# Kernel optimization log

Measured on AMD Instinct MI355X. Metric: run time of the kernel, lower is better.

## Reference

```python
import jax, jax.numpy as jnp
import numpy as np

ALPHA = 1.702   # swiglu_alpha
LIMIT = 7.0     # swiglu_limit
EPS = 1e-5      # norm_eps
E = 16          # num_experts
K = 4           # experts_per_token


def _swiglu(h):
    # interleaved split as in torch: even cols -> glu, odd cols -> linear
    x_glu = jnp.minimum(h[..., ::2], LIMIT)
    # faithful to source bug: clamp(min=limit, max=limit) == constant limit
    x_lin = jnp.clip(h[..., 1::2], LIMIT, LIMIT)
    return x_glu * jax.nn.sigmoid(ALPHA * x_glu) * (x_lin + 1.0)


def setup_inputs() -> dict:
    key = jax.random.key(0)
    ks = jax.random.split(key, 7)
    B, T, H, I = 1, 2048, 1024, 1024
    x = jax.random.normal(ks[0], (B, T, H), jnp.float32)
    scale = jnp.ones((H,), jnp.float32)
    gate_w = jax.random.normal(ks[1], (E, H), jnp.float32) * 0.02
    gate_b = jnp.zeros((E,), jnp.float32)
    mlp1_w = jax.random.normal(ks[2], (E, 2 * I, H), jnp.float32) * 0.02
    mlp1_b = jax.random.normal(ks[3], (E, 2 * I), jnp.float32) * 0.02
    mlp2_w = jax.random.normal(ks[4], (E, H, I), jnp.float32) * 0.02
    mlp2_b = jax.random.normal(ks[5], (E, H), jnp.float32) * 0.02
    return dict(x=x, scale=scale, gate_w=gate_w, gate_b=gate_b,
                mlp1_w=mlp1_w, mlp1_b=mlp1_b, mlp2_w=mlp2_w, mlp2_b=mlp2_b)


def reference(x, scale, gate_w, gate_b, mlp1_w, mlp1_b, mlp2_w, mlp2_b):
    # RMSNorm (fp32 math, identity cast here since inputs are fp32)
    t = x * jax.lax.rsqrt(jnp.mean(x * x, axis=-1, keepdims=True) + EPS) * scale
    # gate + top-k routing (sorted descending, matching torch.topk sorted=True)
    g = jnp.einsum('bth,eh->bte', t, gate_w) + gate_b          # [B,T,E]
    vals, idx = jax.lax.top_k(g, K)                            # [B,T,K]
    w = jax.nn.softmax(vals, axis=-1)                          # [B,T,K]
    # route[b,t,e] = sum_k w[b,t,k] * [idx[b,t,k]==e]  (top-k indices distinct)
    route = jnp.sum(jax.nn.one_hot(idx, E, dtype=t.dtype) * w[..., None], axis=-2)
    route_e = jnp.moveaxis(route, -1, 0)                       # [E,B,T]
    # grouped dense-per-expert computation instead of per-token weight gather:
    # mathematically identical output, avoids materializing [B,T,K,2I,H] gathers
    def step(acc, p):
        w1, b1, w2, b2, r = p
        h = jnp.einsum('bth,ih->bti', t, w1) + b1              # [B,T,2I]
        s = _swiglu(h)                                         # [B,T,I]
        y = jnp.einsum('bti,hi->bth', s, w2) + b2              # [B,T,H]
        return acc + r[..., None] * y, None
    acc, _ = jax.lax.scan(step, jnp.zeros_like(x),
                          (mlp1_w, mlp1_b, mlp2_w, mlp2_b, route_e))
    return x + acc
```

## Files before the change

kernel.cpp:

```cpp
#include <hip/hip_runtime.h>
#include <hip/hip_bf16.h>

typedef __bf16 bf16;
typedef __bf16 bf16x4 __attribute__((ext_vector_type(4)));
typedef __bf16 bf16x8 __attribute__((ext_vector_type(8)));
typedef float f32x4 __attribute__((ext_vector_type(4)));

constexpr int TKN  = 2048;
constexpr int HD   = 1024;
constexpr int NEXP = 16;
constexpr int KSEL = 4;
constexpr int IDIM = 1024;
constexpr int I2   = 2048;
constexpr int NROW = TKN * KSEL;

__device__ __forceinline__ void async_copy16(const void* g, void* l) {
  __builtin_amdgcn_global_load_lds((__attribute__((address_space(1))) void*)g,
                                   (__attribute__((address_space(3))) void*)l,
                                   16, 0, 0);
}

__global__ __launch_bounds__(256) void k_norm_gate(
    const float* __restrict__ x, const float* __restrict__ scale,
    const float* __restrict__ gate_w, const float* __restrict__ gate_b,
    float* __restrict__ out, bf16* __restrict__ tN,
    int* __restrict__ eids, float* __restrict__ wts)
{
  __shared__ float tLds[HD];
  __shared__ float red[4];
  __shared__ float gsh[NEXP];
  const int tid = threadIdx.x;
  const int tok = blockIdx.x;
  const int wid = tid >> 6, lane = tid & 63;

  const float4 x4 = *(const float4*)(x + (size_t)tok * HD + tid * 4);
  float ss = x4.x * x4.x + x4.y * x4.y + x4.z * x4.z + x4.w * x4.w;
  #pragma unroll
  for (int off = 32; off > 0; off >>= 1) ss += __shfl_down(ss, off);
  if (lane == 0) red[wid] = ss;
  __syncthreads();
  ss = red[0] + red[1] + red[2] + red[3];
  const float r = rsqrtf(ss * (1.0f / HD) + 1e-5f);

  const float4 s4 = *(const float4*)(scale + tid * 4);
  float4 t4;
  t4.x = x4.x * r * s4.x; t4.y = x4.y * r * s4.y;
  t4.z = x4.z * r * s4.z; t4.w = x4.w * r * s4.w;
  *(float4*)(out + (size_t)tok * HD + tid * 4) = x4;
  tLds[tid * 4 + 0] = t4.x; tLds[tid * 4 + 1] = t4.y;
  tLds[tid * 4 + 2] = t4.z; tLds[tid * 4 + 3] = t4.w;
  bf16x4 tb;
  tb[0] = (bf16)t4.x; tb[1] = (bf16)t4.y; tb[2] = (bf16)t4.z; tb[3] = (bf16)t4.w;
  *(bf16x4*)(tN + (size_t)tok * HD + tid * 4) = tb;
  __syncthreads();

  {
    const int e = tid >> 4, l16 = tid & 15;
    float p = 0.f;
    const float* gw = gate_w + (size_t)e * HD;
    for (int j = l16; j < HD; j += 16) p += tLds[j] * gw[j];
    p += __shfl_xor(p, 8); p += __shfl_xor(p, 4);
    p += __shfl_xor(p, 2); p += __shfl_xor(p, 1);
    if (l16 == 0) gsh[e] = p + gate_b[e];
  }
  __syncthreads();

  if (tid == 0) {
    float g[NEXP];
    #pragma unroll
    for (int i = 0; i < NEXP; ++i) g[i] = gsh[i];
    int   bi[KSEL]; float bv[KSEL];
    #pragma unroll
    for (int k = 0; k < KSEL; ++k) {
      float best = -1e30f; int b = 0;
      for (int i = 0; i < NEXP; ++i) if (g[i] > best) { best = g[i]; b = i; }
      bv[k] = best; bi[k] = b; g[b] = -1e30f;
    }
    const float m = bv[0];
    float wv[KSEL], sum = 0.f;
    #pragma unroll
    for (int k = 0; k < KSEL; ++k) { wv[k] = __expf(bv[k] - m); sum += wv[k]; }
    const float inv = 1.0f / sum;
    #pragma unroll
    for (int k = 0; k < KSEL; ++k) {
      eids[tok * KSEL + k] = bi[k];
      wts[tok * KSEL + k]  = wv[k] * inv;
    }
  }
}

__global__ __launch_bounds__(256) void k_route(
    const int* __restrict__ eids, const float* __restrict__ wts,
    int* __restrict__ cntg, int* __restrict__ segg,
    int* __restrict__ rowTok, float* __restrict__ rowW)
{
  __shared__ int hcnt[NEXP], hoff[NEXP], hrun[NEXP];
  const int tid = threadIdx.x;
  if (tid < NEXP) { hcnt[tid] = 0; hrun[tid] = 0; }
  __syncthreads();
  for (int i = tid; i < NROW; i += 256) atomicAdd(&hcnt[eids[i]], 1);
  __syncthreads();
  if (tid == 0) {
    int s = 0;
    for (int e = 0; e < NEXP; ++e) { hoff[e] = s; segg[e] = s; cntg[e] = hcnt[e]; s += hcnt[e]; }
  }
  __syncthreads();
  for (int i = tid; i < NROW; i += 256) {
    const int e = eids[i];
    const int slot = atomicAdd(&hrun[e], 1);
    const int row = hoff[e] + slot;
    rowTok[row] = i >> 2;
    rowW[row]   = wts[i];
  }
}

__global__ __launch_bounds__(256) void k_gemm1(
    const bf16* __restrict__ tN, const float* __restrict__ w1,
    const float* __restrict__ b1, const int* __restrict__ cnt,
    const int* __restrict__ segOff, const int* __restrict__ rowTok,
    bf16* __restrict__ sBuf)
{
  const int e = blockIdx.z, mt = blockIdx.y, nt = blockIdx.x;
  const int rows = cnt[e];
  if (mt * 128 >= rows) return;
  const int soff = segOff[e];
  __shared__ __align__(16) bf16 Asm[128 * 32];
  __shared__ __align__(16) bf16 Bsm[128 * 32];
  const int tid = threadIdx.x;
  const int wid = tid >> 6, lane = tid & 63;
  const int quad = lane >> 4, l16 = lane & 15;
  const int wm = wid & 1, wn = wid >> 1;

  const int r0 = wid * 16 + (lane >> 2);
  const int r1 = 64 + r0;
  const int colE = (lane & 3) * 8;
  const int m0 = min(mt * 128 + r0, rows - 1);
  const int m1 = min(mt * 128 + r1, rows - 1);
  const char* gA0 = (const char*)(tN + (size_t)rowTok[soff + m0] * HD + colE);
  const char* gA1 = (const char*)(tN + (size_t)rowTok[soff + m1] * HD + colE);
  bf16* lA0 = Asm + wid * 512;
  bf16* lA1 = Asm + 2048 + wid * 512;

  const int brow = tid >> 3;
  const int bkk  = (tid & 7) * 4;
  const int n0 = nt * 128;
  const float* gB = w1 + (size_t)e * I2 * HD + (size_t)(2 * (n0 + brow)) * HD + bkk;

  const f32x4 zero = {0.f, 0.f, 0.f, 0.f};
  f32x4 acc[4][4];
  #pragma unroll
  for (int i = 0; i < 4; ++i)
    #pragma unroll
    for (int j = 0; j < 4; ++j) acc[i][j] = zero;

  for (int kt = 0; kt < 32; ++kt) {
    async_copy16(gA0, lA0);
    async_copy16(gA1, lA1);
    gA0 += 64; gA1 += 64;
    #pragma unroll
    for (int q = 0; q < 4; ++q) {
      const float4 v = *(const float4*)(gB + (size_t)q * 64 * HD);
      bf16x4 c;
      c[0] = (bf16)v.x; c[1] = (bf16)v.y; c[2] = (bf16)v.z; c[3] = (bf16)v.w;
      *(bf16x4*)(Bsm + (q * 32 + brow) * 32 + bkk) = c;
    }
    gB += 32;
    __syncthreads();
    bf16x8 av[4], bv[4];
    #pragma unroll
    for (int i = 0; i < 4; ++i)
      av[i] = *(const bf16x8*)(Asm + (wm * 64 + i * 16 + l16) * 32 + quad * 8);
    #pragma unroll
    for (int j = 0; j < 4; ++j)
      bv[j] = *(const bf16x8*)(Bsm + (wn * 64 + j * 16 + l16) * 32 + quad * 8);
    #pragma unroll
    for (int i = 0; i < 4; ++i)
      #pragma unroll
      for (int j = 0; j < 4; ++j)
        acc[i][j] = __builtin_amdgcn_mfma_f32_16x16x32_bf16(av[i], bv[j], acc[i][j], 0, 0, 0);
    __syncthreads();
  }

  const int mbase = mt * 128 + wm * 64;
  #pragma unroll
  for (int j = 0; j < 4; ++j) {
    const int ncol = n0 + wn * 64 + j * 16 + l16;
    const float bias = b1[(size_t)e * I2 + 2 * ncol];
    #pragma unroll
    for (int i = 0; i < 4; ++i) {
      #pragma unroll
      for (int rg = 0; rg < 4; ++rg) {
        const int gm = mbase + i * 16 + quad * 4 + rg;
        if (gm < rows) {
          const float h  = acc[i][j][rg] + bias;
          const float xg = fminf(h, 7.0f);
          const float s  = xg * (1.0f / (1.0f + __expf(-1.702f * xg))) * 8.0f;
          sBuf[((size_t)soff + gm) * IDIM + ncol] = (bf16)s;
        }
      }
    }
  }
}

__global__ __launch_bounds__(256) void k_gemm2(
    const bf16* __restrict__ sBuf, const float* __restrict__ w2,
    const float* __restrict__ b2, const int* __restrict__ cnt,
    const int* __restrict__ segOff, const int* __restrict__ rowTok,
    const float* __restrict__ rowW, float* __restrict__ out)
{
  const int e = blockIdx.z, mt = blockIdx.y, nt = blockIdx.x;
  const int rows = cnt[e];
  if (mt * 128 >= rows) return;
  const int soff = segOff[e];
  __shared__ __align__(16) bf16 Asm[128 * 32];
  __shared__ __align__(16) bf16 Bsm[128 * 32];
  const int tid = threadIdx.x;
  const int wid = tid >> 6, lane = tid & 63;
  const int quad = lane >> 4, l16 = lane & 15;
  const int wm = wid & 1, wn = wid >> 1;

  const int r0 = wid * 16 + (lane >> 2);
  const int r1 = 64 + r0;
  const int colE = (lane & 3) * 8;
  const int m0 = min(mt * 128 + r0, rows - 1);
  const int m1 = min(mt * 128 + r1, rows - 1);
  const char* gA0 = (const char*)(sBuf + ((size_t)soff + m0) * IDIM + colE);
  const char* gA1 = (const char*)(sBuf + ((size_t)soff + m1) * IDIM + colE);
  bf16* lA0 = Asm + wid * 512;
  bf16* lA1 = Asm + 2048 + wid * 512;

  const int brow = tid >> 3;
  const int bkk  = (tid & 7) * 4;
  const int n0 = nt * 128;
  const float* gB = w2 + (size_t)e * HD * IDIM + (size_t)(n0 + brow) * IDIM + bkk;

  const f32x4 zero = {0.f, 0.f, 0.f, 0.f};
  f32x4 acc[4][4];
  #pragma unroll
  for (int i = 0; i < 4; ++i)
    #pragma unroll
    for (int j = 0; j < 4; ++j) acc[i][j] = zero;

  for (int kt = 0; kt < 32; ++kt) {
    async_copy16(gA0, lA0);
    async_copy16(gA1, lA1);
    gA0 += 64; gA1 += 64;
    #pragma unroll
    for (int q = 0; q < 4; ++q) {
      const float4 v = *(const float4*)(gB + (size_t)q * 32 * IDIM);
      bf16x4 c;
      c[0] = (bf16)v.x; c[1] = (bf16)v.y; c[2] = (bf16)v.z; c[3] = (bf16)v.w;
      *(bf16x4*)(Bsm + (q * 32 + brow) * 32 + bkk) = c;
    }
    gB += 32;
    __syncthreads();
    bf16x8 av[4], bv[4];
    #pragma unroll
    for (int i = 0; i < 4; ++i)
      av[i] = *(const bf16x8*)(Asm + (wm * 64 + i * 16 + l16) * 32 + quad * 8);
    #pragma unroll
    for (int j = 0; j < 4; ++j)
      bv[j] = *(const bf16x8*)(Bsm + (wn * 64 + j * 16 + l16) * 32 + quad * 8);
    #pragma unroll
    for (int i = 0; i < 4; ++i)
      #pragma unroll
      for (int j = 0; j < 4; ++j)
        acc[i][j] = __builtin_amdgcn_mfma_f32_16x16x32_bf16(av[i], bv[j], acc[i][j], 0, 0, 0);
    __syncthreads();
  }

  const int mbase = mt * 128 + wm * 64;
  #pragma unroll
  for (int j = 0; j < 4; ++j) {
    const int ncol = n0 + wn * 64 + j * 16 + l16;
    const float bias = b2[(size_t)e * HD + ncol];
    #pragma unroll
    for (int i = 0; i < 4; ++i) {
      #pragma unroll
      for (int rg = 0; rg < 4; ++rg) {
        const int gm = mbase + i * 16 + quad * 4 + rg;
        if (gm < rows) {
          const int   tok = rowTok[soff + gm];
          const float wgt = rowW[soff + gm];
          atomicAdd(out + (size_t)tok * HD + ncol, wgt * (acc[i][j][rg] + bias));
        }
      }
    }
  }
}

extern "C" void kernel_launch(void* const* d_in, const int* in_sizes, int n_in,
                              void* d_out, int out_size, void* d_ws, size_t ws_size,
                              hipStream_t stream) {
  const float* x      = (const float*)d_in[0];
  const float* scale  = (const float*)d_in[1];
  const float* gate_w = (const float*)d_in[2];
  const float* gate_b = (const float*)d_in[3];
  const float* w1     = (const float*)d_in[4];
  const float* b1     = (const float*)d_in[5];
  const float* w2     = (const float*)d_in[6];
  const float* b2     = (const float*)d_in[7];
  float* out = (float*)d_out;

  char* p = (char*)d_ws;
  bf16* tN   = (bf16*)p;  p += (size_t)TKN * HD * 2;
  bf16* sBuf = (bf16*)p;  p += (size_t)NROW * IDIM * 2;
  int*   eids   = (int*)p;   p += (size_t)NROW * 4;
  float* wts    = (float*)p; p += (size_t)NROW * 4;
  int*   rowTok = (int*)p;   p += (size_t)NROW * 4;
  float* rowW   = (float*)p; p += (size_t)NROW * 4;
  int*   cntg   = (int*)p;   p += 256;
  int*   segg   = (int*)p;   p += 256;

  k_norm_gate<<<TKN, 256, 0, stream>>>(x, scale, gate_w, gate_b, out, tN, eids, wts);
  k_route<<<1, 256, 0, stream>>>(eids, wts, cntg, segg, rowTok, rowW);
  k_gemm1<<<dim3(8, 16, NEXP), 256, 0, stream>>>(tN, w1, b1, cntg, segg, rowTok, sBuf);
  k_gemm2<<<dim3(8, 16, NEXP), 256, 0, stream>>>(sBuf, w2, b2, cntg, segg, rowTok, rowW, out);
}
```

Baseline: 395.8 us.

## Pre-convert expert weights to bf16 and async-load them into LDS

Adds two conversion kernels that write the used (even) rows of w1 and all of w2 into bf16 copies in the workspace on every call. The grouped GEMMs then load B tiles with the same global-to-LDS async copies used for A, instead of loading fp32 from global memory, converting in registers and storing to LDS. This is meant to halve the weight bytes read by each GEMM tile and remove the conversion and store work from the inner loop. The cost is an extra full pass over the fp32 weights plus bf16 writes, two more kernel launches, and a dependence on the workspace being large enough, with the old path kept as a fallback.

```diff
diff --git a/kernel.cpp b/kernel.cpp
--- a/kernel.cpp
+++ b/kernel.cpp
@@ -114,11 +114,39 @@
   }
 }
 
+__global__ __launch_bounds__(256) void k_cvt_w1(const float* __restrict__ w1,
+                                                bf16* __restrict__ w1b) {
+  const size_t f = (size_t)blockIdx.x * 256 + threadIdx.x;
+  const size_t row = f >> 7;
+  const int    off = (int)(f & 127) * 8;
+  const size_t e = row >> 10, n = row & 1023;
+  const float* s = w1 + (e * 2048 + 2 * n) * 1024 + off;
+  const float4 a = *(const float4*)(s);
+  const float4 b = *(const float4*)(s + 4);
+  bf16x8 o;
+  o[0] = (bf16)a.x; o[1] = (bf16)a.y; o[2] = (bf16)a.z; o[3] = (bf16)a.w;
+  o[4] = (bf16)b.x; o[5] = (bf16)b.y; o[6] = (bf16)b.z; o[7] = (bf16)b.w;
+  *(bf16x8*)(w1b + row * 1024 + off) = o;
+}
+
+__global__ __launch_bounds__(256) void k_cvt_w2(const float* __restrict__ w2,
+                                                bf16* __restrict__ w2b) {
+  const size_t f = (size_t)blockIdx.x * 256 + threadIdx.x;
+  const size_t base = f * 8;
+  const float4 a = *(const float4*)(w2 + base);
+  const float4 b = *(const float4*)(w2 + base + 4);
+  bf16x8 o;
+  o[0] = (bf16)a.x; o[1] = (bf16)a.y; o[2] = (bf16)a.z; o[3] = (bf16)a.w;
+  o[4] = (bf16)b.x; o[5] = (bf16)b.y; o[6] = (bf16)b.z; o[7] = (bf16)b.w;
+  *(bf16x8*)(w2b + base) = o;
+}
+
+template <bool PREP>
 __global__ __launch_bounds__(256) void k_gemm1(
     const bf16* __restrict__ tN, const float* __restrict__ w1,
-    const float* __restrict__ b1, const int* __restrict__ cnt,
-    const int* __restrict__ segOff, const int* __restrict__ rowTok,
-    bf16* __restrict__ sBuf)
+    const bf16* __restrict__ w1b, const float* __restrict__ b1,
+    const int* __restrict__ cnt, const int* __restrict__ segOff,
+    const int* __restrict__ rowTok, bf16* __restrict__ sBuf)
 {
   const int e = blockIdx.z, mt = blockIdx.y, nt = blockIdx.x;
   const int rows = cnt[e];
@@ -141,9 +169,13 @@
   bf16* lA0 = Asm + wid * 512;
   bf16* lA1 = Asm + 2048 + wid * 512;
 
+  const int n0 = nt * 128;
+  const char* gB0 = (const char*)(w1b + (size_t)e * IDIM * HD + (size_t)(n0 + r0) * HD + colE);
+  const char* gB1 = (const char*)(w1b + (size_t)e * IDIM * HD + (size_t)(n0 + r1) * HD + colE);
+  bf16* lB0 = Bsm + wid * 512;
+  bf16* lB1 = Bsm + 2048 + wid * 512;
   const int brow = tid >> 3;
   const int bkk  = (tid & 7) * 4;
-  const int n0 = nt * 128;
   const float* gB = w1 + (size_t)e * I2 * HD + (size_t)(2 * (n0 + brow)) * HD + bkk;
 
   const f32x4 zero = {0.f, 0.f, 0.f, 0.f};
@@ -157,14 +189,20 @@
     async_copy16(gA0, lA0);
     async_copy16(gA1, lA1);
     gA0 += 64; gA1 += 64;
-    #pragma unroll
-    for (int q = 0; q < 4; ++q) {
-      const float4 v = *(const float4*)(gB + (size_t)q * 64 * HD);
-      bf16x4 c;
-      c[0] = (bf16)v.x; c[1] = (bf16)v.y; c[2] = (bf16)v.z; c[3] = (bf16)v.w;
-      *(bf16x4*)(Bsm + (q * 32 + brow) * 32 + bkk) = c;
-    }
-    gB += 32;
+    if constexpr (PREP) {
+      async_copy16(gB0, lB0);
+      async_copy16(gB1, lB1);
+      gB0 += 64; gB1 += 64;
+    } else {
+      #pragma unroll
+      for (int q = 0; q < 4; ++q) {
+        const float4 v = *(const float4*)(gB + (size_t)q * 64 * HD);
+        bf16x4 c;
+        c[0] = (bf16)v.x; c[1] = (bf16)v.y; c[2] = (bf16)v.z; c[3] = (bf16)v.w;
+        *(bf16x4*)(Bsm + (q * 32 + brow) * 32 + bkk) = c;
+      }
+      gB += 32;
+    }
     __syncthreads();
     bf16x8 av[4], bv[4];
     #pragma unroll
@@ -202,11 +240,13 @@
   }
 }
 
+template <bool PREP>
 __global__ __launch_bounds__(256) void k_gemm2(
     const bf16* __restrict__ sBuf, const float* __restrict__ w2,
-    const float* __restrict__ b2, const int* __restrict__ cnt,
-    const int* __restrict__ segOff, const int* __restrict__ rowTok,
-    const float* __restrict__ rowW, float* __restrict__ out)
+    const bf16* __restrict__ w2b, const float* __restrict__ b2,
+    const int* __restrict__ cnt, const int* __restrict__ segOff,
+    const int* __restrict__ rowTok, const float* __restrict__ rowW,
+    float* __restrict__ out)
 {
   const int e = blockIdx.z, mt = blockIdx.y, nt = blockIdx.x;
   const int rows = cnt[e];
@@ -229,9 +269,13 @@
   bf16* lA0 = Asm + wid * 512;
   bf16* lA1 = Asm + 2048 + wid * 512;
 
+  const int n0 = nt * 128;
+  const char* gB0 = (const char*)(w2b + (size_t)e * HD * IDIM + (size_t)(n0 + r0) * IDIM + colE);
+  const char* gB1 = (const char*)(w2b + (size_t)e * HD * IDIM + (size_t)(n0 + r1) * IDIM + colE);
+  bf16* lB0 = Bsm + wid * 512;
+  bf16* lB1 = Bsm + 2048 + wid * 512;
   const int brow = tid >> 3;
   const int bkk  = (tid & 7) * 4;
-  const int n0 = nt * 128;
   const float* gB = w2 + (size_t)e * HD * IDIM + (size_t)(n0 + brow) * IDIM + bkk;
 
   const f32x4 zero = {0.f, 0.f, 0.f, 0.f};
@@ -245,14 +289,20 @@
     async_copy16(gA0, lA0);
     async_copy16(gA1, lA1);
     gA0 += 64; gA1 += 64;
-    #pragma unroll
-    for (int q = 0; q < 4; ++q) {
-      const float4 v = *(const float4*)(gB + (size_t)q * 32 * IDIM);
-      bf16x4 c;
-      c[0] = (bf16)v.x; c[1] = (bf16)v.y; c[2] = (bf16)v.z; c[3] = (bf16)v.w;
-      *(bf16x4*)(Bsm + (q * 32 + brow) * 32 + bkk) = c;
-    }
-    gB += 32;
+    if constexpr (PREP) {
+      async_copy16(gB0, lB0);
+      async_copy16(gB1, lB1);
+      gB0 += 64; gB1 += 64;
+    } else {
+      #pragma unroll
+      for (int q = 0; q < 4; ++q) {
+        const float4 v = *(const float4*)(gB + (size_t)q * 32 * IDIM);
+        bf16x4 c;
+        c[0] = (bf16)v.x; c[1] = (bf16)v.y; c[2] = (bf16)v.z; c[3] = (bf16)v.w;
+        *(bf16x4*)(Bsm + (q * 32 + brow) * 32 + bkk) = c;
+      }
+      gB += 32;
+    }
     __syncthreads();
     bf16x8 av[4], bv[4];
     #pragma unroll
@@ -311,9 +361,25 @@
   float* rowW   = (float*)p; p += (size_t)NROW * 4;
   int*   cntg   = (int*)p;   p += 256;
   int*   segg   = (int*)p;   p += 256;
+  const size_t base_need = (size_t)(p - (char*)d_ws);
+  const size_t WSZ = (size_t)NEXP * IDIM * HD * 2;
+  bf16* w2b = (bf16*)p;
+  bf16* w1b = (bf16*)(p + WSZ);
+  const bool prep2 = ws_size >= base_need + WSZ;
+  const bool prep1 = ws_size >= base_need + 2 * WSZ;
 
   k_norm_gate<<<TKN, 256, 0, stream>>>(x, scale, gate_w, gate_b, out, tN, eids, wts);
   k_route<<<1, 256, 0, stream>>>(eids, wts, cntg, segg, rowTok, rowW);
-  k_gemm1<<<dim3(8, 16, NEXP), 256, 0, stream>>>(tN, w1, b1, cntg, segg, rowTok, sBuf);
-  k_gemm2<<<dim3(8, 16, NEXP), 256, 0, stream>>>(sBuf, w2, b2, cntg, segg, rowTok, rowW, out);
-}
+  if (prep1) k_cvt_w1<<<8192, 256, 0, stream>>>(w1, w1b);
+  if (prep2) k_cvt_w2<<<8192, 256, 0, stream>>>(w2, w2b);
+
+  if (prep1)
+    k_gemm1<true><<<dim3(8, 16, NEXP), 256, 0, stream>>>(tN, w1, w1b, b1, cntg, segg, rowTok, sBuf);
+  else
+    k_gemm1<false><<<dim3(8, 16, NEXP), 256, 0, stream>>>(tN, w1, w1b, b1, cntg, segg, rowTok, sBuf);
+
+  if (prep2)
+    k_gemm2<true><<<dim3(8, 16, NEXP), 256, 0, stream>>>(sBuf, w2, w2b, b2, cntg, segg, rowTok, rowW, out);
+  else
+    k_gemm2<false><<<dim3(8, 16, NEXP), 256, 0, stream>>>(sBuf, w2, w2b, b2, cntg, segg, rowTok, rowW, out);
+}
```

Result: faster. 387.8 us (-2.0%).
